# Performance work log

Measured on AMD Instinct MI355X. Metric: run time of the kernel, lower is better.

Reference implementation:

```python
import jax, jax.numpy as jnp
import numpy as np

NEG_SLOPE = 0.2  # PyG GATConv default LeakyReLU slope
EPS = 1e-16


def gat_conv(x, edge_index, W, a_src, a_dst, bias, heads, out_ch, concat):
    """PyG-style GATConv (eval mode, add_self_loops=True).
    x: [N, F_in], edge_index: [2, E] (row0=source, row1=target).
    """
    N = x.shape[0]
    loops = jnp.arange(N, dtype=edge_index.dtype)
    src = jnp.concatenate([edge_index[0], loops])  # [E+N]
    dst = jnp.concatenate([edge_index[1], loops])

    h = (x @ W).reshape(N, heads, out_ch)            # [N, H, C]
    alpha_s = jnp.sum(h * a_src, axis=-1)            # [N, H]
    alpha_d = jnp.sum(h * a_dst, axis=-1)            # [N, H]

    e = alpha_s[src] + alpha_d[dst]                  # [E+N, H]
    e = jnp.where(e > 0, e, NEG_SLOPE * e)           # LeakyReLU

    # segment softmax over incoming edges of each target node
    m = jax.ops.segment_max(e, dst, num_segments=N)  # [N, H]
    m = jnp.where(jnp.isfinite(m), m, 0.0)
    ex = jnp.exp(e - m[dst])
    s = jax.ops.segment_sum(ex, dst, num_segments=N)  # [N, H]
    alpha = ex / (s[dst] + EPS)                       # [E+N, H]

    msg = h[src] * alpha[:, :, None]                  # [E+N, H, C]
    out = jax.ops.segment_sum(msg, dst, num_segments=N)  # [N, H, C]

    if concat:
        out = out.reshape(N, heads * out_ch)
    else:
        out = out.mean(axis=1)
    return out + bias


def setup_inputs() -> dict:
    key = jax.random.key(0)
    ks = jax.random.split(key, 10)
    N, E, F_in = 50000, 1000000, 128
    H, C, OUT = 4, 16, 40
    x = jax.random.normal(ks[0], (N, F_in), dtype=jnp.float32)
    edge_index = jax.random.randint(ks[1], (2, E), 0, N, dtype=jnp.int64)
    sc1 = 1.0 / np.sqrt(F_in)
    sc2 = 1.0 / np.sqrt(H * C)
    return {
        "x": x,
        "edge_index": edge_index,
        "W1": jax.random.normal(ks[2], (F_in, H * C), dtype=jnp.float32) * sc1,
        "a_src1": jax.random.normal(ks[3], (H, C), dtype=jnp.float32) * sc2,
        "a_dst1": jax.random.normal(ks[4], (H, C), dtype=jnp.float32) * sc2,
        "b1": jnp.zeros((H * C,), dtype=jnp.float32),
        "W2": jax.random.normal(ks[5], (H * C, OUT), dtype=jnp.float32) * sc2,
        "a_src2": jax.random.normal(ks[6], (1, OUT), dtype=jnp.float32) * 0.15,
        "a_dst2": jax.random.normal(ks[7], (1, OUT), dtype=jnp.float32) * 0.15,
        "b2": jnp.zeros((OUT,), dtype=jnp.float32),
    }


def reference(x, edge_index, W1, a_src1, a_dst1, b1, W2, a_src2, a_dst2, b2):
    h = gat_conv(x, edge_index, W1, a_src1, a_dst1, b1, heads=4, out_ch=16, concat=True)
    h = jax.nn.elu(h)  # dropout is identity in eval mode
    out = gat_conv(h, edge_index, W2, a_src2, a_dst2, b2, heads=1, out_ch=40, concat=False)
    return out
```

## Files before the change

### kernel.cpp

```cpp
#include <hip/hip_runtime.h>

#define NEG_SLOPE 0.2f
#define GAT_EPS 1e-16f
#define NB 1024

__device__ __forceinline__ float leaky(float e){ return e > 0.f ? e : NEG_SLOPE * e; }

__device__ __forceinline__ unsigned bf2(float a, float b){
  unsigned ua = __float_as_uint(a); ua += 0x7FFFu + ((ua >> 16) & 1u);
  unsigned ub = __float_as_uint(b); ub += 0x7FFFu + ((ub >> 16) & 1u);
  return (ua >> 16) | (ub & 0xFFFF0000u);
}
__device__ __forceinline__ float bflo(unsigned v){ return __uint_as_float(v << 16); }
__device__ __forceinline__ float bfhi(unsigned v){ return __uint_as_float(v & 0xFFFF0000u); }

__device__ __forceinline__ unsigned long long pick8(int k,
    unsigned long long m0, unsigned long long m1, unsigned long long m2,
    unsigned long long m3, unsigned long long m4, unsigned long long m5,
    unsigned long long m6, unsigned long long m7){
  return k==0?m0:k==1?m1:k==2?m2:k==3?m3:k==4?m4:k==5?m5:k==6?m6:m7;
}

__global__ __launch_bounds__(256) void k_gemm1(const float* __restrict__ x,
                                               const float* __restrict__ W,
                                               const float* __restrict__ a_src,
                                               const float* __restrict__ a_dst,
                                               unsigned* __restrict__ h1b,
                                               float* __restrict__ as1,
                                               float* __restrict__ ad1, int N){
  __shared__ float Ws[128*64];
  __shared__ float xs[64*20];
  const int t = threadIdx.x;
  const int n0 = blockIdx.x * 64;
  for (int i = t; i < 128*64/4; i += 256) ((float4*)Ws)[i] = ((const float4*)W)[i];
  const int ct = t & 15;
  const int rt = t >> 4;
  const int lr = t >> 2;
  const int lq = t & 3;
  const bool rok = (n0 + lr) < N;
  const float* xrow = x + (size_t)(n0 + lr)*128 + lq*4;
  float acc[4][4];
#pragma unroll
  for (int i = 0; i < 4; i++)
#pragma unroll
    for (int j = 0; j < 4; j++) acc[i][j] = 0.f;

  for (int kc = 0; kc < 8; kc++){
    float4 xv = {0.f,0.f,0.f,0.f};
    if (rok) xv = *(const float4*)(xrow + kc*16);
    __syncthreads();
    *(float4*)(xs + lr*20 + lq*4) = xv;
    __syncthreads();
#pragma unroll
    for (int kk = 0; kk < 16; kk++){
      const int k = kc*16 + kk;
      float4 wv = *(const float4*)(Ws + k*64 + ct*4);
      float x0 = xs[(rt*4+0)*20 + kk];
      float x1 = xs[(rt*4+1)*20 + kk];
      float x2 = xs[(rt*4+2)*20 + kk];
      float x3 = xs[(rt*4+3)*20 + kk];
      acc[0][0] += x0*wv.x; acc[0][1] += x0*wv.y; acc[0][2] += x0*wv.z; acc[0][3] += x0*wv.w;
      acc[1][0] += x1*wv.x; acc[1][1] += x1*wv.y; acc[1][2] += x1*wv.z; acc[1][3] += x1*wv.w;
      acc[2][0] += x2*wv.x; acc[2][1] += x2*wv.y; acc[2][2] += x2*wv.z; acc[2][3] += x2*wv.w;
      acc[3][0] += x3*wv.x; acc[3][1] += x3*wv.y; acc[3][2] += x3*wv.z; acc[3][3] += x3*wv.w;
    }
  }
  const int h = ct >> 2;
  const float4 asv = *(const float4*)(a_src + ct*4);
  const float4 adv = *(const float4*)(a_dst + ct*4);
#pragma unroll
  for (int i = 0; i < 4; i++){
    int n = n0 + rt*4 + i;
    float ss = acc[i][0]*asv.x + acc[i][1]*asv.y + acc[i][2]*asv.z + acc[i][3]*asv.w;
    float dd = acc[i][0]*adv.x + acc[i][1]*adv.y + acc[i][2]*adv.z + acc[i][3]*adv.w;
    ss += __shfl_xor(ss, 1); ss += __shfl_xor(ss, 2);
    dd += __shfl_xor(dd, 1); dd += __shfl_xor(dd, 2);
    if (n < N){
      h1b[(size_t)n*32 + ct*2 + 0] = bf2(acc[i][0], acc[i][1]);
      h1b[(size_t)n*32 + ct*2 + 1] = bf2(acc[i][2], acc[i][3]);
      if ((ct & 3) == 0){
        as1[(size_t)n*4 + h] = ss;
        ad1[(size_t)n*4 + h] = dd;
      }
    }
  }
}

__global__ __launch_bounds__(64) void k_cnt(const int* __restrict__ ei,
                                            int* __restrict__ bcnt,
                                            int E, int T, int N, int chunk){
  const int lane = (int)threadIdx.x;
  const int b = blockIdx.x;
  const int lo = b*chunk;
  const int hi = min(lo + chunk, T);
  int cntr = 0;
  for (int base = lo; base < hi; base += 64){
    const int i = base + lane;
    int bin = 8;
    if (i < hi){
      int dst = (i < E) ? ei[E+i] : (i - E);
      bin = (int)(((unsigned)dst * 8u) / (unsigned)N);
    }
    unsigned long long m0=__ballot(bin==0), m1=__ballot(bin==1),
                       m2=__ballot(bin==2), m3=__ballot(bin==3),
                       m4=__ballot(bin==4), m5=__ballot(bin==5),
                       m6=__ballot(bin==6), m7=__ballot(bin==7);
    if (lane < 8) cntr += __popcll(pick8(lane,m0,m1,m2,m3,m4,m5,m6,m7));
  }
  if (lane < 8) bcnt[b*8 + lane] = cntr;
}

__global__ __launch_bounds__(512) void k_scan(const int* __restrict__ bcnt,
                                              int* __restrict__ qbase,
                                              int* __restrict__ qtot){
  const int w = (int)threadIdx.x >> 6;
  const int l = (int)threadIdx.x & 63;
  int vals[NB/64];
  int s = 0;
#pragma unroll
  for (int j = 0; j < NB/64; j++){
    vals[j] = bcnt[((l*(NB/64)) + j)*8 + w];
    s += vals[j];
  }
  int incl = s;
#pragma unroll
  for (int off = 1; off < 64; off <<= 1){
    int t = __shfl_up(incl, off);
    if (l >= off) incl += t;
  }
  int run = incl - s;
#pragma unroll
  for (int j = 0; j < NB/64; j++){
    qbase[((l*(NB/64)) + j)*8 + w] = run;
    run += vals[j];
  }
  if (l == 63) qtot[w] = run;
}

__global__ __launch_bounds__(64) void k_scat(const int* __restrict__ ei,
                                             const int* __restrict__ qbase,
                                             unsigned* __restrict__ queue,
                                             int E, int T, int N, int cap, int chunk){
  const int lane = (int)threadIdx.x;
  const int b = blockIdx.x;
  const int lo = b*chunk;
  const int hi = min(lo + chunk, T);
  int cntr = (lane < 8) ? qbase[b*8 + lane] : 0;
  for (int base = lo; base < hi; base += 64){
    const int i = base + lane;
    int src = 0, dst = 0, bin = 8;
    if (i < hi){
      if (i < E){ src = ei[i]; dst = ei[E+i]; }
      else      { src = dst = i - E; }
      bin = (int)(((unsigned)dst * 8u) / (unsigned)N);
    }
    unsigned long long m0=__ballot(bin==0), m1=__ballot(bin==1),
                       m2=__ballot(bin==2), m3=__ballot(bin==3),
                       m4=__ballot(bin==4), m5=__ballot(bin==5),
                       m6=__ballot(bin==6), m7=__ballot(bin==7);
    int cur = cntr;
    if (lane < 8) cntr += __popcll(pick8(lane,m0,m1,m2,m3,m4,m5,m6,m7));
    const int bb = (bin < 8) ? bin : 0;
    const int mybase = __shfl(cur, bb);
    if (bin < 8){
      unsigned long long mm = pick8(bin,m0,m1,m2,m3,m4,m5,m6,m7);
      const int off = __popcll(mm & ((1ull << lane) - 1ull));
      const int pos = mybase + off;
      if (pos < cap)
        queue[(size_t)bin*cap + pos] = ((unsigned)dst << 16) | (unsigned)src;
    }
  }
}

__global__ __launch_bounds__(256) void k_fillq(const int* __restrict__ qtot,
                                               const unsigned* __restrict__ queue,
                                               int* __restrict__ cnt,
                                               unsigned short* __restrict__ slots,
                                               int cap){
  const int xcd  = blockIdx.x & 7;
  const int grp  = blockIdx.x >> 3;
  const int ngrp = gridDim.x >> 3;
  const int qn = min(qtot[xcd], cap);
  const unsigned* q = queue + (size_t)xcd*cap;
  for (int i = grp*256 + (int)threadIdx.x; i < qn; i += ngrp*256){
    const unsigned p = q[i];
    const int dst = (int)(p >> 16);
    const int pos = atomicAdd(cnt + dst, 1);
    if (pos < 64) slots[(size_t)dst*64 + pos] = (unsigned short)(p & 0xFFFFu);
  }
}

__global__ __launch_bounds__(256) void k_edge1(const int* __restrict__ cnt,
     const unsigned short* __restrict__ slots, const float* __restrict__ as1,
     const float* __restrict__ ad1, const unsigned* __restrict__ h1b,
     const float* __restrict__ b1, float* __restrict__ g1, int N){
  int wave = (blockIdx.x << 2) + (threadIdx.x >> 6);
  if (wave >= N) return;
  const int lane = threadIdx.x & 63;
  const int e8 = lane >> 3;
  const int c8 = lane & 7;
  const int h  = c8 >> 1;
  const int deg = min(cnt[wave], 64);
  const int base = wave << 6;
  const float4 ad = *(const float4*)(ad1 + (size_t)wave*4);
  const float adh = (h==0)?ad.x:(h==1)?ad.y:(h==2)?ad.z:ad.w;

  float4 accA = {0.f,0.f,0.f,0.f};
  float4 accB = {0.f,0.f,0.f,0.f};
  float lsum = 0.f;
  for (int jb = 0; jb < deg; jb += 8){
    int slot = jb + e8;
    int s = 0; float p = 0.f;
    if (slot < deg){
      s = slots[base + slot];
      p = __expf(leaky(as1[(size_t)s*4 + h] + adh));
    }
    uint4 w = *(const uint4*)(h1b + (size_t)s*32 + c8*4);
    accA.x += p * bflo(w.x); accA.y += p * bfhi(w.x);
    accA.z += p * bflo(w.y); accA.w += p * bfhi(w.y);
    accB.x += p * bflo(w.z); accB.y += p * bfhi(w.z);
    accB.z += p * bflo(w.w); accB.w += p * bfhi(w.w);
    lsum += p;
  }
#pragma unroll
  for (int off = 8; off < 64; off <<= 1){
    accA.x += __shfl_xor(accA.x, off); accA.y += __shfl_xor(accA.y, off);
    accA.z += __shfl_xor(accA.z, off); accA.w += __shfl_xor(accA.w, off);
    accB.x += __shfl_xor(accB.x, off); accB.y += __shfl_xor(accB.y, off);
    accB.z += __shfl_xor(accB.z, off); accB.w += __shfl_xor(accB.w, off);
  }
  lsum += __shfl_xor(lsum, 1);
  lsum += __shfl_xor(lsum, 8);
  lsum += __shfl_xor(lsum, 16);
  lsum += __shfl_xor(lsum, 32);
  lsum *= 0.5f;

  if (e8 == 0){
    float inv = 1.f / (lsum + GAT_EPS);
    const float4 bA = *(const float4*)(b1 + c8*8);
    const float4 bB = *(const float4*)(b1 + c8*8 + 4);
    float4 vA, vB;
    vA.x = accA.x*inv + bA.x; vA.y = accA.y*inv + bA.y;
    vA.z = accA.z*inv + bA.z; vA.w = accA.w*inv + bA.w;
    vB.x = accB.x*inv + bB.x; vB.y = accB.y*inv + bB.y;
    vB.z = accB.z*inv + bB.z; vB.w = accB.w*inv + bB.w;
    vA.x = vA.x > 0.f ? vA.x : (__expf(vA.x) - 1.f);
    vA.y = vA.y > 0.f ? vA.y : (__expf(vA.y) - 1.f);
    vA.z = vA.z > 0.f ? vA.z : (__expf(vA.z) - 1.f);
    vA.w = vA.w > 0.f ? vA.w : (__expf(vA.w) - 1.f);
    vB.x = vB.x > 0.f ? vB.x : (__expf(vB.x) - 1.f);
    vB.y = vB.y > 0.f ? vB.y : (__expf(vB.y) - 1.f);
    vB.z = vB.z > 0.f ? vB.z : (__expf(vB.z) - 1.f);
    vB.w = vB.w > 0.f ? vB.w : (__expf(vB.w) - 1.f);
    *(float4*)(g1 + (size_t)wave*64 + c8*8)     = vA;
    *(float4*)(g1 + (size_t)wave*64 + c8*8 + 4) = vB;
  }
}

__global__ __launch_bounds__(256) void k_gemm2(const float* __restrict__ g1,
                                               const float* __restrict__ W2,
                                               const float* __restrict__ a_src,
                                               const float* __restrict__ a_dst,
                                               unsigned* __restrict__ h2lo,
                                               unsigned* __restrict__ h2hi,
                                               float* __restrict__ as2,
                                               float* __restrict__ ad2, int N){
  __shared__ float Ws[64*40];
  __shared__ float xs[32*64];
  const int t = threadIdx.x;
  const int n0 = blockIdx.x * 32;
  for (int i = t; i < 64*40; i += 256) Ws[i] = W2[i];
  for (int i = t; i < 32*64; i += 256){
    int n = n0 + (i >> 6);
    xs[i] = (n < N) ? g1[(size_t)n*64 + (i & 63)] : 0.f;
  }
  __syncthreads();
  const int c  = t & 63;
  const int ng = t >> 6;
  const bool act = (c < 40);
  float acc[8] = {0,0,0,0,0,0,0,0};
  if (act){
    for (int k = 0; k < 64; k++){
      float w = Ws[k*40 + c];
#pragma unroll
      for (int r = 0; r < 8; r++) acc[r] += xs[(ng*8+r)*64 + k] * w;
    }
  }
  const float av = act ? a_src[c] : 0.f;
  const float bv = act ? a_dst[c] : 0.f;
#pragma unroll
  for (int r = 0; r < 8; r++){
    int n = n0 + ng*8 + r;
    float po = __shfl_xor(acc[r], 1);
    if ((c & 1) == 0 && act && n < N){
      unsigned pk = bf2(acc[r], po);
      if (c < 32) h2lo[(size_t)n*16 + (c >> 1)] = pk;
      else        h2hi[(size_t)n*4  + ((c-32) >> 1)] = pk;
    }
    float ss = acc[r]*av, dd = acc[r]*bv;
#pragma unroll
    for (int off = 1; off < 64; off <<= 1){
      ss += __shfl_xor(ss, off);
      dd += __shfl_xor(dd, off);
    }
    if (c == 0 && n < N){ as2[n] = ss; ad2[n] = dd; }
  }
}

__global__ __launch_bounds__(256) void k_edge2(const int* __restrict__ cnt,
     const unsigned short* __restrict__ slots, const float* __restrict__ as2,
     const float* __restrict__ ad2, const unsigned* __restrict__ h2lo,
     const unsigned* __restrict__ h2hi, const float* __restrict__ b2,
     float* __restrict__ out, int N){
  int wave = (blockIdx.x << 2) + (threadIdx.x >> 6);
  if (wave >= N) return;
  const int lane = threadIdx.x & 63;
  const int e8 = lane >> 3;
  const int c8 = lane & 7;
  const int deg = min(cnt[wave], 64);
  const int base = wave << 6;
  const float adw = ad2[wave];

  float4 accA = {0.f,0.f,0.f,0.f};
  float4 accB = {0.f,0.f,0.f,0.f};
  float lsum = 0.f;
  for (int jb = 0; jb < deg; jb += 8){
    int slot = jb + e8;
    int s = 0; float p = 0.f;
    if (slot < deg){
      s = slots[base + slot];
      p = __expf(leaky(as2[s] + adw));
    }
    lsum += p;
    if (c8 < 5){
      uint4 w = (c8 < 4) ? *(const uint4*)(h2lo + (size_t)s*16 + c8*4)
                         : *(const uint4*)(h2hi + (size_t)s*4);
      accA.x += p * bflo(w.x); accA.y += p * bfhi(w.x);
      accA.z += p * bflo(w.y); accA.w += p * bfhi(w.y);
      accB.x += p * bflo(w.z); accB.y += p * bfhi(w.z);
      accB.z += p * bflo(w.w); accB.w += p * bfhi(w.w);
    }
  }
#pragma unroll
  for (int off = 8; off < 64; off <<= 1){
    accA.x += __shfl_xor(accA.x, off); accA.y += __shfl_xor(accA.y, off);
    accA.z += __shfl_xor(accA.z, off); accA.w += __shfl_xor(accA.w, off);
    accB.x += __shfl_xor(accB.x, off); accB.y += __shfl_xor(accB.y, off);
    accB.z += __shfl_xor(accB.z, off); accB.w += __shfl_xor(accB.w, off);
  }
#pragma unroll
  for (int off = 1; off < 64; off <<= 1) lsum += __shfl_xor(lsum, off);
  lsum *= 0.125f;

  if (e8 == 0 && c8 < 5){
    float inv = 1.f / (lsum + GAT_EPS);
    const float4 bA = *(const float4*)(b2 + c8*8);
    const float4 bB = *(const float4*)(b2 + c8*8 + 4);
    float4 vA, vB;
    vA.x = accA.x*inv + bA.x; vA.y = accA.y*inv + bA.y;
    vA.z = accA.z*inv + bA.z; vA.w = accA.w*inv + bA.w;
    vB.x = accB.x*inv + bB.x; vB.y = accB.y*inv + bB.y;
    vB.z = accB.z*inv + bB.z; vB.w = accB.w*inv + bB.w;
    *(float4*)(out + (size_t)wave*40 + c8*8)     = vA;
    *(float4*)(out + (size_t)wave*40 + c8*8 + 4) = vB;
  }
}

extern "C" void kernel_launch(void* const* d_in, const int* in_sizes, int n_in,
                              void* d_out, int out_size, void* d_ws, size_t ws_size,
                              hipStream_t stream){
  const float* x    = (const float*)d_in[0];
  const int*   ei   = (const int*)d_in[1];
  const float* W1   = (const float*)d_in[2];
  const float* a_s1 = (const float*)d_in[3];
  const float* a_d1 = (const float*)d_in[4];
  const float* b1   = (const float*)d_in[5];
  const float* W2   = (const float*)d_in[6];
  const float* a_s2 = (const float*)d_in[7];
  const float* a_d2 = (const float*)d_in[8];
  const float* b2   = (const float*)d_in[9];
  float* out = (float*)d_out;

  const int N = in_sizes[0] / 128;
  const int E = in_sizes[1] / 2;
  const int T = E + N;
  const int cap = T/8 + 65536;
  const int chunk = (T + NB - 1)/NB;

  float* ws = (float*)d_ws;
  unsigned* h1b  = (unsigned*)ws; ws += (size_t)N*32;
  unsigned* h2lo = (unsigned*)ws; ws += (size_t)N*16;
  unsigned* h2hi = (unsigned*)ws; ws += (size_t)N*4;
  float* as1 = ws;  ws += (size_t)N*4;
  float* ad1 = ws;  ws += (size_t)N*4;
  float* g1  = ws;  ws += (size_t)N*64;
  float* as2 = ws;  ws += (size_t)N;
  float* ad2 = ws;  ws += (size_t)N;
  int* cnt   = (int*)ws;          ws += (size_t)N;
  int* bcnt  = (int*)ws;          ws += (size_t)NB*8;
  int* qbase = (int*)ws;          ws += (size_t)NB*8;
  int* qtot  = (int*)ws;          ws += 8;
  unsigned short* slots = (unsigned short*)ws; ws += (size_t)N*32;
  unsigned* queue = (unsigned*)ws; ws += (size_t)cap*8;

  hipMemsetAsync(cnt, 0, (size_t)N*sizeof(int), stream);
  hipLaunchKernelGGL(k_cnt,  dim3(NB), dim3(64),  0, stream, ei, bcnt, E, T, N, chunk);
  hipLaunchKernelGGL(k_scan, dim3(1),  dim3(512), 0, stream, bcnt, qbase, qtot);
  hipLaunchKernelGGL(k_scat, dim3(NB), dim3(64),  0, stream, ei, qbase, queue, E, T, N, cap, chunk);
  hipLaunchKernelGGL(k_fillq, dim3(2048), dim3(256), 0, stream, qtot, queue, cnt, slots, cap);

  hipLaunchKernelGGL(k_gemm1, dim3((N+63)/64), dim3(256), 0, stream,
                     x, W1, a_s1, a_d1, h1b, as1, ad1, N);
  hipLaunchKernelGGL(k_edge1, dim3((N+3)/4), dim3(256), 0, stream,
                     cnt, slots, as1, ad1, h1b, b1, g1, N);

  hipLaunchKernelGGL(k_gemm2, dim3((N+31)/32), dim3(256), 0, stream,
                     g1, W2, a_s2, a_d2, h2lo, h2hi, as2, ad2, N);
  hipLaunchKernelGGL(k_edge2, dim3((N+3)/4), dim3(256), 0, stream,
                     cnt, slots, as2, ad2, h2lo, h2hi, b2, out, N);
}
```

Baseline: 281.4 us.

## Replace global atomic slot fill with per-block LDS counters over destination ranges

k_fillq now gives each block a fixed range of 128 destination nodes within one bin. The block scans that bin's whole queue with vectorized uint4 loads, keeps only edges whose target falls in its range, and counts them with shared-memory atomics. The local counts are then written to cnt directly, so the memset and the global atomics on cnt go away. The cost is that every block re-reads its entire bin queue, so total queue traffic grows by roughly the number of groups per bin. cap is rounded to a multiple of 1024 so the vector loads stay aligned.

```diff
diff --git a/kernel.cpp b/kernel.cpp
--- a/kernel.cpp
+++ b/kernel.cpp
@@ -3,6 +3,7 @@
 #define NEG_SLOPE 0.2f
 #define GAT_EPS 1e-16f
 #define NB 1024
+#define DPB 128
 
 __device__ __forceinline__ float leaky(float e){ return e > 0.f ? e : NEG_SLOPE * e; }
 
@@ -176,17 +177,45 @@
                                                const unsigned* __restrict__ queue,
                                                int* __restrict__ cnt,
                                                unsigned short* __restrict__ slots,
-                                               int cap){
-  const int xcd  = blockIdx.x & 7;
-  const int grp  = blockIdx.x >> 3;
-  const int ngrp = gridDim.x >> 3;
-  const int qn = min(qtot[xcd], cap);
-  const unsigned* q = queue + (size_t)xcd*cap;
-  for (int i = grp*256 + (int)threadIdx.x; i < qn; i += ngrp*256){
+                                               int cap, int N){
+  __shared__ int lcnt[DPB];
+  const int bin = blockIdx.x & 7;
+  const int grp = blockIdx.x >> 3;
+  const int binLo = (int)(((long long)N * bin) >> 3);
+  const int binHi = (int)(((long long)N * (bin+1)) >> 3);
+  const int lo = binLo + grp*DPB;
+  if (lo >= binHi) return;
+  const int hi = min(lo + DPB, binHi);
+  for (int i = threadIdx.x; i < DPB; i += 256) lcnt[i] = 0;
+  __syncthreads();
+  const int qn = min(qtot[bin], cap);
+  const unsigned* q = queue + (size_t)bin*cap;
+  const int nv = qn >> 2;
+  const uint4* q4 = (const uint4*)q;
+  for (int i = (int)threadIdx.x; i < nv; i += 256){
+    const uint4 v = q4[i];
+#pragma unroll
+    for (int j = 0; j < 4; j++){
+      const unsigned p = (j==0)?v.x:(j==1)?v.y:(j==2)?v.z:v.w;
+      const int dst = (int)(p >> 16);
+      if (dst >= lo && dst < hi){
+        const int pos = atomicAdd(&lcnt[dst - lo], 1);
+        if (pos < 64) slots[(size_t)dst*64 + pos] = (unsigned short)(p & 0xFFFFu);
+      }
+    }
+  }
+  for (int i = (nv << 2) + (int)threadIdx.x; i < qn; i += 256){
     const unsigned p = q[i];
     const int dst = (int)(p >> 16);
-    const int pos = atomicAdd(cnt + dst, 1);
-    if (pos < 64) slots[(size_t)dst*64 + pos] = (unsigned short)(p & 0xFFFFu);
+    if (dst >= lo && dst < hi){
+      const int pos = atomicAdd(&lcnt[dst - lo], 1);
+      if (pos < 64) slots[(size_t)dst*64 + pos] = (unsigned short)(p & 0xFFFFu);
+    }
+  }
+  __syncthreads();
+  for (int i = threadIdx.x; i < DPB; i += 256){
+    const int d = lo + i;
+    if (d < hi) cnt[d] = lcnt[i];
   }
 }
 
@@ -384,8 +413,9 @@
   const int N = in_sizes[0] / 128;
   const int E = in_sizes[1] / 2;
   const int T = E + N;
-  const int cap = T/8 + 65536;
+  const int cap = ((T/8 + 65536) + 1023) & ~1023;
   const int chunk = (T + NB - 1)/NB;
+  const int G = (((N + 7)/8) + DPB - 1)/DPB;
 
   float* ws = (float*)d_ws;
   unsigned* h1b  = (unsigned*)ws; ws += (size_t)N*32;
@@ -403,11 +433,10 @@
   unsigned short* slots = (unsigned short*)ws; ws += (size_t)N*32;
   unsigned* queue = (unsigned*)ws; ws += (size_t)cap*8;
 
-  hipMemsetAsync(cnt, 0, (size_t)N*sizeof(int), stream);
   hipLaunchKernelGGL(k_cnt,  dim3(NB), dim3(64),  0, stream, ei, bcnt, E, T, N, chunk);
   hipLaunchKernelGGL(k_scan, dim3(1),  dim3(512), 0, stream, bcnt, qbase, qtot);
   hipLaunchKernelGGL(k_scat, dim3(NB), dim3(64),  0, stream, ei, qbase, queue, E, T, N, cap, chunk);
-  hipLaunchKernelGGL(k_fillq, dim3(2048), dim3(256), 0, stream, qtot, queue, cnt, slots, cap);
+  hipLaunchKernelGGL(k_fillq, dim3(8*G), dim3(256), 0, stream, qtot, queue, cnt, slots, cap, N);
 
   hipLaunchKernelGGL(k_gemm1, dim3((N+63)/64), dim3(256), 0, stream,
                      x, W1, a_s1, a_d1, h1b, as1, ad1, N);
```

Measured after the change: 299.1 us. 1.06x slower.
